# Kernel tuning notes

Hardware: AMD Instinct MI355X
Metric: run time of the kernel (lower is better)

## Reference

```python
import jax, jax.numpy as jnp
import numpy as np

B, DIM, S = 8, 512, 1024
H, DH = 8, 64
FF_INNER = 1024      # dim * (ff_mult//2)
CONV_INNER = 1024    # dim * expansion_factor
K = 31
PAD = (K - 1) // 2


def _bn(x, g, b):
    # eval-mode BatchNorm2d with running stats (0,1) absorbed: per-channel affine
    return x * g[None, :, None, None] + b[None, :, None, None]


def _pw(x, w, b):
    # 1x1 Conv2d == channel matmul. x: [B,C,S,1], w: [O,C]
    return jnp.einsum('oc,bcst->bost', w, x) + b[None, :, None, None]


def _ff(x, g, b, w1, b1, w2, b2):
    h = _pw(_bn(x, g, b), w1, b1)
    return _pw(jax.nn.silu(h), w2, b2)


def _attn(x, g, b, wq, bq, wk, bk, wv, bv, wo, bo):
    xn = _bn(x, g, b)
    q = _pw(xn, wq, bq)[..., 0].reshape(B, H, DH, S)
    k = _pw(xn, wk, bk)[..., 0].reshape(B, H, DH, S)
    v = _pw(xn, wv, bv)[..., 0].reshape(B, H, DH, S)
    scale = DH ** -0.5
    scores = jnp.einsum('bhds,bhdt->bhst', q, k) * scale   # [B,H,S,S]
    w = jax.nn.softmax(scores, axis=-1)
    o = jnp.einsum('bhst,bhdt->bhds', w, v).reshape(B, H * DH, S)[..., None]
    return _pw(o, wo, bo)


def _conv(x, g, b, pw1_w, pw1_b, dconv_w, dconv_b, cbn_g, cbn_b, pw2_w, pw2_b):
    h = _pw(_bn(x, g, b), pw1_w, pw1_b)          # [B,2*CONV_INNER,S,1]
    a, gate = jnp.split(h, 2, axis=1)
    h = a * jax.nn.sigmoid(gate)                  # GLU
    h = jnp.transpose(h, (0, 1, 3, 2))            # [B,C,1,S] so kernel (1,K) runs along seq
    h = jax.lax.conv_general_dilated(
        h, dconv_w, window_strides=(1, 1), padding=((0, 0), (PAD, PAD)),
        dimension_numbers=('NCHW', 'OIHW', 'NCHW'))
    h = jnp.transpose(h, (0, 1, 3, 2)) + dconv_b[None, :, None, None]
    h = jax.nn.silu(_bn(h, cbn_g, cbn_b))
    return _pw(h, pw2_w, pw2_b)


def setup_inputs() -> dict:
    key = jax.random.key(0)
    ks = iter(jax.random.split(key, 32))
    w = lambda *s: jax.random.normal(next(ks), s, jnp.float32) * 0.02
    d = {
        'x': jax.random.normal(next(ks), (B, DIM, S, 1), jnp.float32),
        'ff1_g': jnp.ones((DIM,)), 'ff1_b': jnp.zeros((DIM,)),
        'ff1_w1': w(FF_INNER, DIM), 'ff1_b1': jnp.zeros((FF_INNER,)),
        'ff1_w2': w(DIM, FF_INNER), 'ff1_b2': jnp.zeros((DIM,)),
        'attn_g': jnp.ones((DIM,)), 'attn_b': jnp.zeros((DIM,)),
        'wq': w(H * DH, DIM), 'bq': jnp.zeros((H * DH,)),
        'wk': w(H * DH, DIM), 'bk': jnp.zeros((H * DH,)),
        'wv': w(H * DH, DIM), 'bv': jnp.zeros((H * DH,)),
        'wo': w(DIM, H * DH), 'bo': jnp.zeros((DIM,)),
        'conv_g': jnp.ones((DIM,)), 'conv_b': jnp.zeros((DIM,)),
        'pw1_w': w(2 * CONV_INNER, DIM), 'pw1_b': jnp.zeros((2 * CONV_INNER,)),
        'dconv_w': w(CONV_INNER, CONV_INNER, 1, K), 'dconv_b': jnp.zeros((CONV_INNER,)),
        'cbn_g': jnp.ones((CONV_INNER,)), 'cbn_b': jnp.zeros((CONV_INNER,)),
        'pw2_w': w(DIM, CONV_INNER), 'pw2_b': jnp.zeros((DIM,)),
        'ff2_g': jnp.ones((DIM,)), 'ff2_b': jnp.zeros((DIM,)),
        'ff2_w1': w(FF_INNER, DIM), 'ff2_b1': jnp.zeros((FF_INNER,)),
        'ff2_w2': w(DIM, FF_INNER), 'ff2_b2': jnp.zeros((DIM,)),
        'fin_g': jnp.ones((DIM,)), 'fin_b': jnp.zeros((DIM,)),
    }
    return d


def reference(x, ff1_g, ff1_b, ff1_w1, ff1_b1, ff1_w2, ff1_b2,
              attn_g, attn_b, wq, bq, wk, bk, wv, bv, wo, bo,
              conv_g, conv_b, pw1_w, pw1_b, dconv_w, dconv_b, cbn_g, cbn_b, pw2_w, pw2_b,
              ff2_g, ff2_b, ff2_w1, ff2_b1, ff2_w2, ff2_b2, fin_g, fin_b):
    x1 = x + 0.5 * _ff(x, ff1_g, ff1_b, ff1_w1, ff1_b1, ff1_w2, ff1_b2)
    x2 = x1 + _attn(x1, attn_g, attn_b, wq, bq, wk, bk, wv, bv, wo, bo)
    x3 = x2 + _conv(x2, conv_g, conv_b, pw1_w, pw1_b, dconv_w, dconv_b, cbn_g, cbn_b, pw2_w, pw2_b)
    x4 = x3 + 0.5 * _ff(x3, ff2_g, ff2_b, ff2_w1, ff2_b1, ff2_w2, ff2_b2)
    return _bn(x4, fin_g, fin_b)
```

## Files before the change

kernel.cpp:

```cpp
#include <hip/hip_runtime.h>
#include <cstdint>
#include <cstddef>

using bf16 = __bf16;
typedef __bf16 bf16x8 __attribute__((ext_vector_type(8)));
typedef float f32x4 __attribute__((ext_vector_type(4)));
typedef unsigned int uint4v __attribute__((ext_vector_type(4)));

#define NB 8
#define DIM 512
#define SEQ 1024
#define NH 8
#define DH 64
#define CONV_INNER 1024
#define KW 31
#define PADW 15
#define HPRA 1056

__device__ __forceinline__ float fsigmoid(float x) { return 1.f / (1.f + __expf(-x)); }
__device__ __forceinline__ float fsilu(float x) { return x * fsigmoid(x); }

__device__ __forceinline__ void gld16(const bf16* g, bf16* l) {
  __builtin_amdgcn_global_load_lds(
      (const __attribute__((address_space(1))) unsigned int*)g,
      (__attribute__((address_space(3))) unsigned int*)l, 16, 0, 0);
}


__global__ __launch_bounds__(256) void k_diag(float* __restrict__ out, int n, float v) {
  int i = blockIdx.x * 256 + threadIdx.x;
  if (i < n) out[i] = v;
}


__global__ __launch_bounds__(256) void k_convert_bf16(const float* __restrict__ src,
                                                      bf16* __restrict__ dst, int n) {
  int i = (blockIdx.x * 256 + threadIdx.x) * 4;
  if (i + 3 < n) {
    float4 v = *reinterpret_cast<const float4*>(src + i);
    dst[i]     = (bf16)v.x;
    dst[i + 1] = (bf16)v.y;
    dst[i + 2] = (bf16)v.z;
    dst[i + 3] = (bf16)v.w;
  }
}

__global__ __launch_bounds__(256) void k_conv_wt(const float* __restrict__ w,
                                                 bf16* __restrict__ wt) {
  __shared__ float t[256 * KW];
  int o = blockIdx.x, i0 = blockIdx.y * 256;
  const float* src = w + (size_t)o * (CONV_INNER * KW) + (size_t)i0 * KW;
  for (int idx = threadIdx.x; idx < 256 * KW; idx += 256) t[idx] = src[idx];
  __syncthreads();
  for (int k = 0; k < KW; ++k) {
    wt[((size_t)k * CONV_INNER + o) * CONV_INNER + i0 + threadIdx.x] =
        (bf16)t[threadIdx.x * KW + k];
  }
}

__global__ __launch_bounds__(256) void k_pad_zero(bf16* __restrict__ hpad) {
  int i = blockIdx.x * 256 + threadIdx.x;
  int b = i / (32 * 128);
  int r = (i >> 7) & 31;
  int c8 = (i & 127) * 8;
  int row = (r < PADW) ? r : 1024 + r;
  uint4v z = {0u, 0u, 0u, 0u};
  *reinterpret_cast<uint4v*>(&hpad[((size_t)b * HPRA + row) * CONV_INNER + c8]) = z;
}

__global__ __launch_bounds__(256) void k_transpose_in(const float* __restrict__ x,
                                                      const float* __restrict__ g,
                                                      const float* __restrict__ bvec,
                                                      float* __restrict__ xT,
                                                      bf16* __restrict__ xbn) {
  __shared__ float t[32][33];
  int s0 = blockIdx.x * 32, c0 = blockIdx.y * 32, b = blockIdx.z;
  int col = threadIdx.x & 31, rq = threadIdx.x >> 5;
#pragma unroll
  for (int i = 0; i < 4; ++i) {
    int row = rq + i * 8;
    t[row][col] = x[((size_t)b * DIM + c0 + row) * SEQ + s0 + col];
  }
  __syncthreads();
  float gg = g[c0 + col], bb = bvec[c0 + col];
#pragma unroll
  for (int i = 0; i < 4; ++i) {
    int srow = rq + i * 8;
    float v = t[col][srow];
    size_t off = ((size_t)b * SEQ + s0 + srow) * DIM + c0 + col;
    xT[off] = v;
    xbn[off] = (bf16)(v * gg + bb);
  }
}

__global__ __launch_bounds__(256) void k_concat_bias(const float* __restrict__ bq,
                                                     const float* __restrict__ bk,
                                                     const float* __restrict__ bv,
                                                     float* __restrict__ qb) {
  int i = blockIdx.x * 256 + threadIdx.x;
  if (i < 512) qb[i] = bq[i];
  else if (i < 1024) qb[i] = bk[i - 512];
  else if (i < 1536) qb[i] = bv[i - 1024];
}

template <int EPI>
__global__ __launch_bounds__(256) void k_gemm(const bf16* __restrict__ A,
                                              const bf16* __restrict__ W,
                                              const float* __restrict__ bias,
                                              const float* __restrict__ res,
                                              const float* __restrict__ g,
                                              const float* __restrict__ bb,
                                              float* __restrict__ outf,
                                              bf16* __restrict__ outb, int N, int K) {
  __shared__ __align__(16) bf16 sA[128][40];
  __shared__ __align__(16) bf16 sB[128][40];
  const int tid = threadIdx.x;
  const int b = blockIdx.z;
  const int m0 = blockIdx.y * 128, n0 = blockIdx.x * 128;
  const int lane = tid & 63, wid = tid >> 6;
  const int wm = (wid & 1) * 64, wn = (wid >> 1) * 64;
  const int fr = lane & 15, fg = lane >> 4;

  f32x4 acc[4][4];
#pragma unroll
  for (int i = 0; i < 4; ++i)
#pragma unroll
    for (int j = 0; j < 4; ++j) acc[i][j] = (f32x4)0.f;

  const int srow = tid >> 1, sc = (tid & 1) * 16;
  const bf16* Abase = A + ((size_t)b * SEQ + m0 + srow) * K + sc;
  const bf16* Wbase = W + (size_t)(n0 + srow) * K + sc;

  for (int kt = 0; kt < K; kt += 32) {
    uint4v a0 = *reinterpret_cast<const uint4v*>(Abase + kt);
    uint4v a1 = *reinterpret_cast<const uint4v*>(Abase + kt + 8);
    uint4v w0 = *reinterpret_cast<const uint4v*>(Wbase + kt);
    uint4v w1 = *reinterpret_cast<const uint4v*>(Wbase + kt + 8);
    *reinterpret_cast<uint4v*>(&sA[srow][sc]) = a0;
    *reinterpret_cast<uint4v*>(&sA[srow][sc + 8]) = a1;
    *reinterpret_cast<uint4v*>(&sB[srow][sc]) = w0;
    *reinterpret_cast<uint4v*>(&sB[srow][sc + 8]) = w1;
    __syncthreads();
    bf16x8 aF[4], bF[4];
#pragma unroll
    for (int i = 0; i < 4; ++i) {
      aF[i] = *reinterpret_cast<const bf16x8*>(&sA[wm + i * 16 + fr][fg * 8]);
      bF[i] = *reinterpret_cast<const bf16x8*>(&sB[wn + i * 16 + fr][fg * 8]);
    }
#pragma unroll
    for (int mi = 0; mi < 4; ++mi)
#pragma unroll
      for (int ni = 0; ni < 4; ++ni)
        acc[mi][ni] =
            __builtin_amdgcn_mfma_f32_16x16x32_bf16(aF[mi], bF[ni], acc[mi][ni], 0, 0, 0);
    __syncthreads();
  }

#pragma unroll
  for (int mi = 0; mi < 4; ++mi) {
#pragma unroll
    for (int ni = 0; ni < 4; ++ni) {
      int ncol = n0 + wn + ni * 16 + fr;
      float bv = bias[ncol];
      if constexpr (EPI == 5) {
        float gg = g[ncol], bbv = bb[ncol];
        int mrow0 = m0 + wm + mi * 16 + fg * 4;
        float v[4];
#pragma unroll
        for (int j = 0; j < 4; ++j) {
          float a = acc[mi][ni][j] + bv;
          float r = res[((size_t)b * SEQ + mrow0 + j) * 512 + ncol] + 0.5f * a;
          v[j] = r * gg + bbv;
        }
        *reinterpret_cast<float4*>(outf + ((size_t)b * 512 + ncol) * SEQ + mrow0) =
            make_float4(v[0], v[1], v[2], v[3]);
      } else {
#pragma unroll
        for (int j = 0; j < 4; ++j) {
          int mrow = m0 + wm + mi * 16 + fg * 4 + j;
          size_t off = ((size_t)b * SEQ + mrow) * N + ncol;
          float a = acc[mi][ni][j] + bv;
          if constexpr (EPI == 0) {
            outb[off] = (bf16)fsilu(a);
          } else if constexpr (EPI == 2) {
            outb[off] = (bf16)a;
          } else if constexpr (EPI == 1) {
            float r = res[off] + 0.5f * a;
            outf[off] = r;
            outb[off] = (bf16)(r * g[ncol] + bb[ncol]);
          } else if constexpr (EPI == 3) {
            float r = res[off] + a;
            outf[off] = r;
            outb[off] = (bf16)(r * g[ncol] + bb[ncol]);
          }
        }
      }
    }
  }
}

__global__ __launch_bounds__(256) void k_pw1_glu(const bf16* __restrict__ A,
                                                 const bf16* __restrict__ W,
                                                 const float* __restrict__ bias,
                                                 bf16* __restrict__ hpad) {
  __shared__ __align__(16) bf16 sA[128][40];
  __shared__ __align__(16) bf16 sBa[128][40];
  __shared__ __align__(16) bf16 sBg[128][40];
  const int tid = threadIdx.x;
  const int b = blockIdx.z;
  const int m0 = blockIdx.y * 128, n0 = blockIdx.x * 128;
  const int lane = tid & 63, wid = tid >> 6;
  const int wm = (wid & 1) * 64, wn = (wid >> 1) * 64;
  const int fr = lane & 15, fg = lane >> 4;
  const int K = 512;

  f32x4 accA[4][4], accG[4][4];
#pragma unroll
  for (int i = 0; i < 4; ++i)
#pragma unroll
    for (int j = 0; j < 4; ++j) { accA[i][j] = (f32x4)0.f; accG[i][j] = (f32x4)0.f; }

  const int srow = tid >> 1, sc = (tid & 1) * 16;
  const bf16* Abase = A + ((size_t)b * SEQ + m0 + srow) * K + sc;
  const bf16* WaB = W + (size_t)(n0 + srow) * K + sc;
  const bf16* WgB = W + (size_t)(n0 + 1024 + srow) * K + sc;

  for (int kt = 0; kt < K; kt += 32) {
    uint4v a0 = *reinterpret_cast<const uint4v*>(Abase + kt);
    uint4v a1 = *reinterpret_cast<const uint4v*>(Abase + kt + 8);
    uint4v wa0 = *reinterpret_cast<const uint4v*>(WaB + kt);
    uint4v wa1 = *reinterpret_cast<const uint4v*>(WaB + kt + 8);
    uint4v wg0 = *reinterpret_cast<const uint4v*>(WgB + kt);
    uint4v wg1 = *reinterpret_cast<const uint4v*>(WgB + kt + 8);
    *reinterpret_cast<uint4v*>(&sA[srow][sc]) = a0;
    *reinterpret_cast<uint4v*>(&sA[srow][sc + 8]) = a1;
    *reinterpret_cast<uint4v*>(&sBa[srow][sc]) = wa0;
    *reinterpret_cast<uint4v*>(&sBa[srow][sc + 8]) = wa1;
    *reinterpret_cast<uint4v*>(&sBg[srow][sc]) = wg0;
    *reinterpret_cast<uint4v*>(&sBg[srow][sc + 8]) = wg1;
    __syncthreads();
    bf16x8 aF[4], bFa[4], bFg[4];
#pragma unroll
    for (int i = 0; i < 4; ++i) {
      aF[i]  = *reinterpret_cast<const bf16x8*>(&sA[wm + i * 16 + fr][fg * 8]);
      bFa[i] = *reinterpret_cast<const bf16x8*>(&sBa[wn + i * 16 + fr][fg * 8]);
      bFg[i] = *reinterpret_cast<const bf16x8*>(&sBg[wn + i * 16 + fr][fg * 8]);
    }
#pragma unroll
    for (int mi = 0; mi < 4; ++mi)
#pragma unroll
      for (int ni = 0; ni < 4; ++ni) {
        accA[mi][ni] =
            __builtin_amdgcn_mfma_f32_16x16x32_bf16(aF[mi], bFa[ni], accA[mi][ni], 0, 0, 0);
        accG[mi][ni] =
            __builtin_amdgcn_mfma_f32_16x16x32_bf16(aF[mi], bFg[ni], accG[mi][ni], 0, 0, 0);
      }
    __syncthreads();
  }

#pragma unroll
  for (int mi = 0; mi < 4; ++mi) {
#pragma unroll
    for (int ni = 0; ni < 4; ++ni) {
      int ncol = n0 + wn + ni * 16 + fr;
      float ba = bias[ncol], bg = bias[ncol + 1024];
#pragma unroll
      for (int j = 0; j < 4; ++j) {
        int mrow = m0 + wm + mi * 16 + fg * 4 + j;
        float av = accA[mi][ni][j] + ba;
        float gv = accG[mi][ni][j] + bg;
        hpad[((size_t)b * HPRA + PADW + mrow) * CONV_INNER + ncol] =
            (bf16)(av * fsigmoid(gv));
      }
    }
  }
}

__global__ __launch_bounds__(256) void k_conv(const bf16* __restrict__ hpad,
                                              const bf16* __restrict__ wt,
                                              const float* __restrict__ bias,
                                              const float* __restrict__ g,
                                              const float* __restrict__ bb,
                                              bf16* __restrict__ outb) {
  __shared__ __align__(16) bf16 sA[160 * 32];
  __shared__ __align__(16) bf16 sB0[64 * 32];
  __shared__ __align__(16) bf16 sB1[64 * 32];
  const int tid = threadIdx.x;
  const int b = blockIdx.z;
  const int n0 = blockIdx.x * 64, m0 = blockIdx.y * 128;
  const int lane = tid & 63, wid = tid >> 6;
  const int wm = (wid & 1) * 64, wn = (wid >> 1) * 32;
  const int fr = lane & 15, fg = lane >> 4;
  const int crow = lane >> 2;
  const int ccol = (((lane & 3) ^ (crow & 3)) * 8);

  f32x4 acc[4][2];
#pragma unroll
  for (int i = 0; i < 4; ++i)
#pragma unroll
    for (int j = 0; j < 2; ++j) acc[i][j] = (f32x4)0.f;

  const bf16* Abase = hpad + ((size_t)b * HPRA + m0 + crow) * CONV_INNER + ccol;
  const bf16* Wbase = wt + (size_t)(n0 + wid * 16 + crow) * CONV_INNER + ccol;

  for (int it = 0; it < 32; ++it) {
    const int itc = it * 32;
#pragma unroll
    for (int c = 0; c < 3; ++c) {
      const int ch = wid + c * 4;
      if (ch < 10)
        gld16(Abase + (size_t)(ch * 16) * CONV_INNER + itc, &sA[ch * 512]);
    }
    gld16(Wbase + itc, &sB0[wid * 512]);
    __syncthreads();

    for (int ks = 0; ks < KW; ++ks) {
      const bf16* cur = (ks & 1) ? sB1 : sB0;
      bf16* nxt = (ks & 1) ? sB0 : sB1;
      if (ks + 1 < KW)
        gld16(Wbase + (size_t)(ks + 1) * CONV_INNER * CONV_INNER + itc, &nxt[wid * 512]);
      bf16x8 aF[4], bF[2];
#pragma unroll
      for (int i = 0; i < 4; ++i) {
        const int ar = ks + wm + i * 16 + fr;
        aF[i] = *reinterpret_cast<const bf16x8*>(&sA[ar * 32 + ((fg ^ (ar & 3)) * 8)]);
      }
#pragma unroll
      for (int n = 0; n < 2; ++n) {
        const int br = wn + n * 16 + fr;
        bF[n] = *reinterpret_cast<const bf16x8*>(&cur[br * 32 + ((fg ^ (br & 3)) * 8)]);
      }
#pragma unroll
      for (int mi = 0; mi < 4; ++mi)
#pragma unroll
        for (int ni = 0; ni < 2; ++ni)
          acc[mi][ni] =
              __builtin_amdgcn_mfma_f32_16x16x32_bf16(aF[mi], bF[ni], acc[mi][ni], 0, 0, 0);
      __syncthreads();
    }
  }

#pragma unroll
  for (int mi = 0; mi < 4; ++mi) {
#pragma unroll
    for (int ni = 0; ni < 2; ++ni) {
      int ncol = n0 + wn + ni * 16 + fr;
      float bv = bias[ncol], gg = g[ncol], bbv = bb[ncol];
#pragma unroll
      for (int j = 0; j < 4; ++j) {
        int mrow = m0 + wm + mi * 16 + fg * 4 + j;
        float a = acc[mi][ni][j] + bv;
        outb[((size_t)b * SEQ + mrow) * CONV_INNER + ncol] = (bf16)fsilu(a * gg + bbv);
      }
    }
  }
}

__global__ __launch_bounds__(256) void k_attn(const bf16* __restrict__ qkv,
                                              bf16* __restrict__ out) {
  __shared__ __align__(16) bf16 sQ[128][72];
  __shared__ __align__(16) bf16 sK[64][72];
  __shared__ __align__(16) bf16 sVT[64][72];
  __shared__ __align__(16) bf16 sP[128][72];
  const int tid = threadIdx.x;
  const int bh = blockIdx.y;
  const int b = bh >> 3, h = bh & 7;
  const int m0 = blockIdx.x * 128;
  const int lane = tid & 63, wid = tid >> 6;
  const int w32 = wid * 32;
  const int fr = lane & 15, fg = lane >> 4;
  const size_t base = (size_t)b * SEQ * 1536;

  for (int idx = tid; idx < 128 * 8; idx += 256) {
    int row = idx >> 3, c = (idx & 7) * 8;
    *reinterpret_cast<uint4v*>(&sQ[row][c]) =
        *reinterpret_cast<const uint4v*>(qkv + base + (size_t)(m0 + row) * 1536 + h * 64 + c);
  }

  f32x4 o[2][4];
  float mst[2][4], lst[2][4];
#pragma unroll
  for (int mi = 0; mi < 2; ++mi)
#pragma unroll
    for (int j = 0; j < 4; ++j) {
      mst[mi][j] = -1e30f;
      lst[mi][j] = 0.f;
#pragma unroll
      for (int df = 0; df < 4; ++df) o[mi][df] = (f32x4)0.f;
    }

  for (int t0 = 0; t0 < SEQ; t0 += 64) {
    for (int idx = tid; idx < 64 * 8; idx += 256) {
      int row = idx >> 3, c = (idx & 7) * 8;
      *reinterpret_cast<uint4v*>(&sK[row][c]) = *reinterpret_cast<const uint4v*>(
          qkv + base + (size_t)(t0 + row) * 1536 + 512 + h * 64 + c);
    }
    for (int e = tid; e < 64 * 64; e += 256) {
      int t = e >> 6, d = e & 63;
      sVT[d][t] = qkv[base + (size_t)(t0 + t) * 1536 + 1024 + h * 64 + d];
    }
    __syncthreads();

    f32x4 sacc[2][4];
#pragma unroll
    for (int mi = 0; mi < 2; ++mi)
#pragma unroll
      for (int tf = 0; tf < 4; ++tf) sacc[mi][tf] = (f32x4)0.f;
#pragma unroll
    for (int kk = 0; kk < 2; ++kk) {
      bf16x8 aQ[2], bK[4];
#pragma unroll
      for (int mi = 0; mi < 2; ++mi)
        aQ[mi] = *reinterpret_cast<const bf16x8*>(&sQ[w32 + mi * 16 + fr][kk * 32 + fg * 8]);
#pragma unroll
      for (int tf = 0; tf < 4; ++tf)
        bK[tf] = *reinterpret_cast<const bf16x8*>(&sK[tf * 16 + fr][kk * 32 + fg * 8]);
#pragma unroll
      for (int mi = 0; mi < 2; ++mi)
#pragma unroll
        for (int tf = 0; tf < 4; ++tf)
          sacc[mi][tf] =
              __builtin_amdgcn_mfma_f32_16x16x32_bf16(aQ[mi], bK[tf], sacc[mi][tf], 0, 0, 0);
    }

#pragma unroll
    for (int mi = 0; mi < 2; ++mi) {
#pragma unroll
      for (int j = 0; j < 4; ++j) {
        float rm = -1e30f;
#pragma unroll
        for (int tf = 0; tf < 4; ++tf) rm = fmaxf(rm, sacc[mi][tf][j] * 0.125f);
#pragma unroll
        for (int off = 1; off < 16; off <<= 1) rm = fmaxf(rm, __shfl_xor(rm, off));
        float mnew = fmaxf(mst[mi][j], rm);
        float al = __expf(mst[mi][j] - mnew);
        float ps = 0.f;
#pragma unroll
        for (int tf = 0; tf < 4; ++tf) {
          float p = __expf(sacc[mi][tf][j] * 0.125f - mnew);
          ps += p;
          sP[w32 + mi * 16 + fg * 4 + j][tf * 16 + fr] = (bf16)p;
        }
#pragma unroll
        for (int off = 1; off < 16; off <<= 1) ps += __shfl_xor(ps, off);
        lst[mi][j] = lst[mi][j] * al + ps;
        mst[mi][j] = mnew;
#pragma unroll
        for (int df = 0; df < 4; ++df) o[mi][df][j] *= al;
      }
    }
    __syncthreads();

#pragma unroll
    for (int kk = 0; kk < 2; ++kk) {
      bf16x8 aP[2], bV[4];
#pragma unroll
      for (int mi = 0; mi < 2; ++mi)
        aP[mi] = *reinterpret_cast<const bf16x8*>(&sP[w32 + mi * 16 + fr][kk * 32 + fg * 8]);
#pragma unroll
      for (int df = 0; df < 4; ++df)
        bV[df] = *reinterpret_cast<const bf16x8*>(&sVT[df * 16 + fr][kk * 32 + fg * 8]);
#pragma unroll
      for (int mi = 0; mi < 2; ++mi)
#pragma unroll
        for (int df = 0; df < 4; ++df)
          o[mi][df] = __builtin_amdgcn_mfma_f32_16x16x32_bf16(aP[mi], bV[df], o[mi][df], 0, 0, 0);
    }
    __syncthreads();
  }

#pragma unroll
  for (int mi = 0; mi < 2; ++mi)
#pragma unroll
    for (int df = 0; df < 4; ++df)
#pragma unroll
      for (int j = 0; j < 4; ++j) {
        int row = m0 + w32 + mi * 16 + fg * 4 + j;
        int col = h * 64 + df * 16 + fr;
        out[((size_t)b * SEQ + row) * 512 + col] = (bf16)(o[mi][df][j] / lst[mi][j]);
      }
}


extern "C" void kernel_launch(void* const* d_in, const int* in_sizes, int n_in,
                              void* d_out, int out_size, void* d_ws, size_t ws_size,
                              hipStream_t stream) {
  const float* x      = (const float*)d_in[0];
  const float* ff1_g  = (const float*)d_in[1];
  const float* ff1_b  = (const float*)d_in[2];
  const float* ff1_w1 = (const float*)d_in[3];
  const float* ff1_b1 = (const float*)d_in[4];
  const float* ff1_w2 = (const float*)d_in[5];
  const float* ff1_b2 = (const float*)d_in[6];
  const float* attn_g = (const float*)d_in[7];
  const float* attn_b = (const float*)d_in[8];
  const float* wq     = (const float*)d_in[9];
  const float* bq     = (const float*)d_in[10];
  const float* wk     = (const float*)d_in[11];
  const float* bk     = (const float*)d_in[12];
  const float* wv     = (const float*)d_in[13];
  const float* bv     = (const float*)d_in[14];
  const float* wo     = (const float*)d_in[15];
  const float* bo     = (const float*)d_in[16];
  const float* conv_g = (const float*)d_in[17];
  const float* conv_b = (const float*)d_in[18];
  const float* pw1_w  = (const float*)d_in[19];
  const float* pw1_b  = (const float*)d_in[20];
  const float* dconv_w = (const float*)d_in[21];
  const float* dconv_b = (const float*)d_in[22];
  const float* cbn_g  = (const float*)d_in[23];
  const float* cbn_b  = (const float*)d_in[24];
  const float* pw2_w  = (const float*)d_in[25];
  const float* pw2_b  = (const float*)d_in[26];
  const float* ff2_g  = (const float*)d_in[27];
  const float* ff2_b  = (const float*)d_in[28];
  const float* ff2_w1 = (const float*)d_in[29];
  const float* ff2_b1 = (const float*)d_in[30];
  const float* ff2_w2 = (const float*)d_in[31];
  const float* ff2_b2 = (const float*)d_in[32];
  const float* fin_g  = (const float*)d_in[33];
  const float* fin_b  = (const float*)d_in[34];

  char* ws = (char*)d_ws;
  size_t off = 0;
  auto alloc = [&](size_t bytes) -> void* {
    off = (off + 255) & ~(size_t)255;
    void* p = ws + off;
    off += bytes;
    return p;
  };

  bf16* wqkv  = (bf16*)alloc((size_t)1536 * 512 * 2);
  float* qkvb = (float*)alloc(1536 * 4);
  bf16* wf1a  = (bf16*)alloc((size_t)1024 * 512 * 2);
  bf16* wf1b  = (bf16*)alloc((size_t)512 * 1024 * 2);
  bf16* wwo   = (bf16*)alloc((size_t)512 * 512 * 2);
  bf16* wpw1  = (bf16*)alloc((size_t)2048 * 512 * 2);
  bf16* wpw2  = (bf16*)alloc((size_t)512 * 1024 * 2);
  bf16* wf2a  = (bf16*)alloc((size_t)1024 * 512 * 2);
  bf16* wf2b  = (bf16*)alloc((size_t)512 * 1024 * 2);

  bf16*  Bn  = (bf16*)alloc((size_t)NB * SEQ * 512 * 2);
  float* F1  = (float*)alloc((size_t)NB * SEQ * 512 * 4);
  bf16*  HGp = (bf16*)alloc((size_t)NB * HPRA * 1024 * 2);
  bf16*  H2  = (bf16*)alloc((size_t)NB * SEQ * 1024 * 2);

  char* E = (char*)alloc((size_t)KW * 1024 * 1024 * 2);
  bf16*  wt     = (bf16*)E;
  bf16*  h1     = (bf16*)E;
  bf16*  qkv    = (bf16*)E;
  bf16*  attn_o = (bf16*)(E + (size_t)24 * 1024 * 1024);
  float* x1     = (float*)(E + (size_t)32 * 1024 * 1024);
  float* x3     = (float*)E;
  bf16*  h3     = (bf16*)(E + (size_t)16 * 1024 * 1024);

  float* xT = F1;
  float* x2 = F1;
  bf16* xbn = Bn, *x1bn = Bn, *x2bn = Bn, *x3bn = Bn;
  size_t needed = off;
  (void)in_sizes; (void)n_in;

  if (ws_size < needed) {
    k_diag<<<(out_size + 255) / 256, 256, 0, stream>>>(
        (float*)d_out, out_size, (float)(ws_size >> 20));
    return;
  }

  auto cvt = [&](const float* s, bf16* d, int n) {
    k_convert_bf16<<<n / 1024, 256, 0, stream>>>(s, d, n);
  };
  cvt(wq, wqkv, 512 * 512);
  cvt(wk, wqkv + 512 * 512, 512 * 512);
  cvt(wv, wqkv + 1024 * 512, 512 * 512);
  cvt(ff1_w1, wf1a, 1024 * 512);
  cvt(ff1_w2, wf1b, 512 * 1024);
  cvt(wo, wwo, 512 * 512);
  cvt(pw1_w, wpw1, 2048 * 512);
  cvt(pw2_w, wpw2, 512 * 1024);
  cvt(ff2_w1, wf2a, 1024 * 512);
  cvt(ff2_w2, wf2b, 512 * 1024);
  k_concat_bias<<<6, 256, 0, stream>>>(bq, bk, bv, qkvb);
  k_pad_zero<<<(NB * 32 * 128) / 256, 256, 0, stream>>>(HGp);
  k_transpose_in<<<dim3(32, 16, NB), 256, 0, stream>>>(x, ff1_g, ff1_b, xT, xbn);

  k_gemm<0><<<dim3(8, 8, NB), 256, 0, stream>>>(xbn, wf1a, ff1_b1, nullptr, nullptr,
                                                nullptr, nullptr, h1, 1024, 512);
  k_gemm<1><<<dim3(4, 8, NB), 256, 0, stream>>>(h1, wf1b, ff1_b2, xT, attn_g, attn_b,
                                                x1, x1bn, 512, 1024);
  k_gemm<2><<<dim3(12, 8, NB), 256, 0, stream>>>(x1bn, wqkv, qkvb, nullptr, nullptr,
                                                 nullptr, nullptr, qkv, 1536, 512);
  k_attn<<<dim3(8, 64), 256, 0, stream>>>(qkv, attn_o);
  k_gemm<3><<<dim3(4, 8, NB), 256, 0, stream>>>(attn_o, wwo, bo, x1, conv_g, conv_b,
                                                x2, x2bn, 512, 512);
  k_conv_wt<<<dim3(1024, 4), 256, 0, stream>>>(dconv_w, wt);
  k_pw1_glu<<<dim3(8, 8, NB), 256, 0, stream>>>(x2bn, wpw1, pw1_b, HGp);
  k_conv<<<dim3(16, 8, NB), 256, 0, stream>>>(HGp, wt, dconv_b, cbn_g, cbn_b, H2);
  k_gemm<3><<<dim3(4, 8, NB), 256, 0, stream>>>(H2, wpw2, pw2_b, x2, ff2_g, ff2_b,
                                                x3, x3bn, 512, 1024);
  k_gemm<0><<<dim3(8, 8, NB), 256, 0, stream>>>(x3bn, wf2a, ff2_b1, nullptr, nullptr,
                                                nullptr, nullptr, h3, 1024, 512);
  k_gemm<5><<<dim3(4, 8, NB), 256, 0, stream>>>(h3, wf2b, ff2_b2, x3, fin_g, fin_b,
                                                (float*)d_out, nullptr, 512, 1024);
}
```

Measured before the change: 896.4 us.

## Enlarge dense conv tile to 128x128 with K=64 chunks and wider swizzle

The full (non-depthwise) 31-tap convolution kernel now uses a 128-column output tile per block instead of 64, and a 64-wide reduction chunk instead of 32. It halves the grid and the number of outer iterations. Each wave computes a 64x64 sub-tile with 16 MFMA accumulators, and the LDS swizzle is widened to 8 groups. The aim is more MFMA work per LDS load and per barrier, and fewer reloads of the input rows. In exchange it uses more registers and LDS (about 52KB), which may lower occupancy.

```diff
diff --git a/kernel.cpp b/kernel.cpp
--- a/kernel.cpp
+++ b/kernel.cpp
@@ -282,60 +282,76 @@
                                               const float* __restrict__ g,
                                               const float* __restrict__ bb,
                                               bf16* __restrict__ outb) {
-  __shared__ __align__(16) bf16 sA[160 * 32];
-  __shared__ __align__(16) bf16 sB0[64 * 32];
-  __shared__ __align__(16) bf16 sB1[64 * 32];
+  __shared__ __align__(16) bf16 sA[160 * 64];
+  __shared__ __align__(16) bf16 sB0[128 * 64];
+  __shared__ __align__(16) bf16 sB1[128 * 64];
   const int tid = threadIdx.x;
   const int b = blockIdx.z;
-  const int n0 = blockIdx.x * 64, m0 = blockIdx.y * 128;
+  const int n0 = blockIdx.x * 128, m0 = blockIdx.y * 128;
   const int lane = tid & 63, wid = tid >> 6;
-  const int wm = (wid & 1) * 64, wn = (wid >> 1) * 32;
+  const int wm = (wid & 1) * 64, wn = (wid >> 1) * 64;
   const int fr = lane & 15, fg = lane >> 4;
-  const int crow = lane >> 2;
-  const int ccol = (((lane & 3) ^ (crow & 3)) * 8);
-
-  f32x4 acc[4][2];
+  const int srow = lane >> 3;
+  const int scol = ((lane & 7) ^ srow) * 8;
+
+  f32x4 acc[4][4];
 #pragma unroll
   for (int i = 0; i < 4; ++i)
 #pragma unroll
-    for (int j = 0; j < 2; ++j) acc[i][j] = (f32x4)0.f;
-
-  const bf16* Abase = hpad + ((size_t)b * HPRA + m0 + crow) * CONV_INNER + ccol;
-  const bf16* Wbase = wt + (size_t)(n0 + wid * 16 + crow) * CONV_INNER + ccol;
-
-  for (int it = 0; it < 32; ++it) {
-    const int itc = it * 32;
-#pragma unroll
-    for (int c = 0; c < 3; ++c) {
+    for (int j = 0; j < 4; ++j) acc[i][j] = (f32x4)0.f;
+
+  const bf16* Abase = hpad + ((size_t)b * HPRA + m0 + srow) * CONV_INNER + scol;
+  const bf16* Wbase = wt + (size_t)(n0 + srow) * CONV_INNER + scol;
+
+  for (int it = 0; it < 16; ++it) {
+    const int itc = it * 64;
+#pragma unroll
+    for (int c = 0; c < 5; ++c) {
       const int ch = wid + c * 4;
-      if (ch < 10)
-        gld16(Abase + (size_t)(ch * 16) * CONV_INNER + itc, &sA[ch * 512]);
-    }
-    gld16(Wbase + itc, &sB0[wid * 512]);
+      gld16(Abase + (size_t)(ch * 8) * CONV_INNER + itc, &sA[ch * 512]);
+    }
+#pragma unroll
+    for (int c = 0; c < 4; ++c) {
+      const int ch = wid + c * 4;
+      gld16(Wbase + (size_t)(ch * 8) * CONV_INNER + itc, &sB0[ch * 512]);
+    }
     __syncthreads();
 
     for (int ks = 0; ks < KW; ++ks) {
       const bf16* cur = (ks & 1) ? sB1 : sB0;
       bf16* nxt = (ks & 1) ? sB0 : sB1;
-      if (ks + 1 < KW)
-        gld16(Wbase + (size_t)(ks + 1) * CONV_INNER * CONV_INNER + itc, &nxt[wid * 512]);
-      bf16x8 aF[4], bF[2];
-#pragma unroll
-      for (int i = 0; i < 4; ++i) {
-        const int ar = ks + wm + i * 16 + fr;
-        aF[i] = *reinterpret_cast<const bf16x8*>(&sA[ar * 32 + ((fg ^ (ar & 3)) * 8)]);
-      }
-#pragma unroll
-      for (int n = 0; n < 2; ++n) {
-        const int br = wn + n * 16 + fr;
-        bF[n] = *reinterpret_cast<const bf16x8*>(&cur[br * 32 + ((fg ^ (br & 3)) * 8)]);
-      }
-#pragma unroll
-      for (int mi = 0; mi < 4; ++mi)
-#pragma unroll
-        for (int ni = 0; ni < 2; ++ni)
-          acc[mi][ni] =
-              __builtin_amdgcn_mfma_f32_16x16x32_bf16(aF[mi], bF[ni], acc[mi][ni], 0, 0, 0);
+      if (ks + 1 < KW) {
+#pragma unroll
+        for (int c = 0; c < 4; ++c) {
+          const int ch = wid + c * 4;
+          gld16(Wbase + (size_t)(ks + 1) * CONV_INNER * CONV_INNER +
+                    (size_t)(ch * 8) * CONV_INNER + itc,
+                &nxt[ch * 512]);
+        }
+      }
+#pragma unroll
+      for (int kk = 0; kk < 2; ++kk) {
+        const int cg = kk * 4 + fg;
+        bf16x8 aF[4], bF[4];
+#pragma unroll
+        for (int i = 0; i < 4; ++i) {
+          const int ar = ks + wm + i * 16 + fr;
+          aF[i] = *reinterpret_cast<const bf16x8*>(
+              &sA[ar * 64 + ((cg ^ (ar & 7)) * 8)]);
+        }
+#pragma unroll
+        for (int n = 0; n < 4; ++n) {
+          const int br = wn + n * 16 + fr;
+          bF[n] = *reinterpret_cast<const bf16x8*>(
+              &cur[br * 64 + ((cg ^ (br & 7)) * 8)]);
+        }
+#pragma unroll
+        for (int mi = 0; mi < 4; ++mi)
+#pragma unroll
+          for (int ni = 0; ni < 4; ++ni)
+            acc[mi][ni] = __builtin_amdgcn_mfma_f32_16x16x32_bf16(aF[mi], bF[ni],
+                                                                  acc[mi][ni], 0, 0, 0);
+      }
       __syncthreads();
     }
   }
@@ -343,7 +359,7 @@
 #pragma unroll
   for (int mi = 0; mi < 4; ++mi) {
 #pragma unroll
-    for (int ni = 0; ni < 2; ++ni) {
+    for (int ni = 0; ni < 4; ++ni) {
       int ncol = n0 + wn + ni * 16 + fr;
       float bv = bias[ncol], gg = g[ncol], bbv = bb[ncol];
 #pragma unroll
@@ -594,7 +610,7 @@
                                                 x2, x2bn, 512, 512);
   k_conv_wt<<<dim3(1024, 4), 256, 0, stream>>>(dconv_w, wt);
   k_pw1_glu<<<dim3(8, 8, NB), 256, 0, stream>>>(x2bn, wpw1, pw1_b, HGp);
-  k_conv<<<dim3(16, 8, NB), 256, 0, stream>>>(HGp, wt, dconv_b, cbn_g, cbn_b, H2);
+  k_conv<<<dim3(8, 8, NB), 256, 0, stream>>>(HGp, wt, dconv_b, cbn_g, cbn_b, H2);
   k_gemm<3><<<dim3(4, 8, NB), 256, 0, stream>>>(H2, wpw2, pw2_b, x2, ff2_g, ff2_b,
                                                 x3, x3bn, 512, 1024);
   k_gemm<0><<<dim3(8, 8, NB), 256, 0, stream>>>(x3bn, wf2a, ff2_b1, nullptr, nullptr,
```

Measured after the change: 818.3 us. 8.7% less time.
